# Optimization experiments

Measured on AMD Instinct MI355X. Metric: run time of the kernel, lower is better.

The kernel has to match this reference:

```python
import jax, jax.numpy as jnp
import numpy as np

B, T_ENC, T_DEC, E = 16, 512, 128, 512
H = 1024


def setup_inputs() -> dict:
    key = jax.random.key(0)
    ks = jax.random.split(key, 16)
    def rn(k, shape, s=0.02):
        return jax.random.normal(k, shape, jnp.float32) * s
    z = lambda *s: jnp.zeros(s, jnp.float32)
    return {
        "inputs": jax.random.normal(ks[0], (B, T_ENC, E), jnp.float32),
        "padded_mels": jax.random.normal(ks[1], (B, 80, T_DEC), jnp.float32),
        "W_enc": rn(ks[2], (128, E)),
        "W_q": rn(ks[3], (128, H)),
        "W_loc_conv": rn(ks[4], (32, 1, 31)),
        "b_loc_conv": z(32),
        "W_loc_dense": rn(ks[5], (128, 32)),
        "b_loc_dense": z(128),
        "w_e": rn(ks[6], (1, 128)),
        "b_e": z(1),
        "W_p1": rn(ks[7], (256, 80)),
        "W_p2": rn(ks[8], (256, 256)),
        "W_ih1": rn(ks[9], (4 * H, 256 + E)),
        "W_hh1": rn(ks[10], (4 * H, H)),
        "b_ih1": z(4 * H),
        "b_hh1": z(4 * H),
        "W_ih2": rn(ks[11], (4 * H, H)),
        "W_hh2": rn(ks[12], (4 * H, H)),
        "b_ih2": z(4 * H),
        "b_hh2": z(4 * H),
        "W_proj": rn(ks[13], (80, H + E)),
        "b_proj": z(80),
        "W_stop": rn(ks[14], (1, H + E)),
        "b_stop": z(1),
    }


def _lstm_cell(x, h, c, W_ih, W_hh, b_ih, b_hh):
    g = W_ih @ x + b_ih + W_hh @ h + b_hh
    i, f, gg, o = jnp.split(g, 4)  # torch gate order: i, f, g, o
    c = jax.nn.sigmoid(f) * c + jax.nn.sigmoid(i) * jnp.tanh(gg)
    h = jax.nn.sigmoid(o) * jnp.tanh(c)
    return h, c


def _forward(inputs, padded_mels, W_enc, W_q, W_loc_conv, b_loc_conv,
             W_loc_dense, b_loc_dense, w_e, b_e, W_p1, W_p2,
             W_ih1, W_hh1, b_ih1, b_hh1, W_ih2, W_hh2, b_ih2, b_hh2,
             W_proj, b_proj, W_stop, b_stop):
    proc_enc = inputs @ W_enc.T  # (B, T_enc, 128)
    # prepend zero frame, use frames 0..T_dec-1 as teacher-forced inputs
    prev = jnp.concatenate([jnp.zeros((B, 80, 1), inputs.dtype), padded_mels], axis=-1)[:, :, :T_DEC]
    prev = jnp.transpose(prev, (2, 0, 1))  # (T_dec, B, 80)
    # F.dropout(p=0.5) in source defaults to training=True -> always applied; deterministic masks here
    mk = jax.random.key(42)
    m1 = jax.random.bernoulli(jax.random.fold_in(mk, 0), 0.5, (T_DEC, B, 256)).astype(inputs.dtype) * 2.0
    m2 = jax.random.bernoulli(jax.random.fold_in(mk, 1), 0.5, (T_DEC, B, 256)).astype(inputs.dtype) * 2.0

    def lstm2(x_seq):
        # faithful to source: (B,1,768) fed to batch_first=False nn.LSTM ->
        # sequence runs over the batch dim with batch=1 and zero init state each step
        zv = jnp.zeros((H,), x_seq.dtype)
        def cell(carry, x):
            h1, c1, h2, c2 = carry
            h1, c1 = _lstm_cell(x, h1, c1, W_ih1, W_hh1, b_ih1, b_hh1)
            h2, c2 = _lstm_cell(h1, h2, c2, W_ih2, W_hh2, b_ih2, b_hh2)
            return (h1, c1, h2, c2), h2
        _, hs = jax.lax.scan(cell, (zv, zv, zv, zv), x_seq)
        return hs  # (B, 1024)

    def step(carry, xs):
        cum, ctx = carry  # (B, T_enc), (B, E)
        x, d1, d2 = xs
        p = jax.nn.relu(x @ W_p1.T) * d1
        p = jax.nn.relu(p @ W_p2.T) * d2
        h = lstm2(jnp.concatenate([p, ctx], axis=-1))  # (B, 1024)
        q = h @ W_q.T  # (B, 128)
        loc = jax.lax.conv_general_dilated(
            cum[:, None, :], W_loc_conv, (1,), [(15, 15)],
            dimension_numbers=("NCH", "OIH", "NCH")) + b_loc_conv[None, :, None]  # (B, 32, T_enc)
        loc = jnp.transpose(loc, (0, 2, 1)) @ W_loc_dense.T + b_loc_dense  # (B, T_enc, 128)
        e = jnp.tanh(q[:, None, :] + loc + proc_enc) @ w_e[0] + b_e[0]  # (B, T_enc)
        aw = jax.nn.softmax(e, axis=1)
        new_ctx = jnp.einsum("bt,bte->be", aw, inputs)  # (B, E)
        do = jnp.concatenate([h, new_ctx], axis=-1)  # (B, 1536)
        frame = do @ W_proj.T + b_proj  # (B, 80)
        stop = do @ W_stop[0] + b_stop[0]  # (B,)
        return (cum + aw, new_ctx), (frame, stop)

    carry0 = (jnp.zeros((B, T_ENC), inputs.dtype), jnp.zeros((B, E), inputs.dtype))
    _, (mels, stops) = jax.lax.scan(step, carry0, (prev, m1, m2))
    return jnp.transpose(mels, (1, 0, 2)), jnp.transpose(stops, (1, 0))


def reference(inputs, padded_mels, W_enc, W_q, W_loc_conv, b_loc_conv,
              W_loc_dense, b_loc_dense, w_e, b_e, W_p1, W_p2,
              W_ih1, W_hh1, b_ih1, b_hh1, W_ih2, W_hh2, b_ih2, b_hh2,
              W_proj, b_proj, W_stop, b_stop):
    return _forward(inputs, padded_mels, W_enc, W_q, W_loc_conv, b_loc_conv,
                    W_loc_dense, b_loc_dense, w_e, b_e, W_p1, W_p2,
                    W_ih1, W_hh1, b_ih1, b_hh1, W_ih2, W_hh2, b_ih2, b_hh2,
                    W_proj, b_proj, W_stop, b_stop)
```

## Files before the change

kernel.cpp:

```cpp
#include <hip/hip_runtime.h>
#include <hip/hip_bf16.h>
#include <stdint.h>

#define TD 128
#define NB 16
#define TE 512
#define EE 512
#define HH 1024
#define NM 80
#define PP 256
#define NWG 256
#define NTH 512

#define AGENT __HIP_MEMORY_SCOPE_AGENT

__device__ inline float aloadf(const float* p) {
  return __hip_atomic_load(p, __ATOMIC_RELAXED, AGENT);
}
__device__ inline void astoref(float* p, float v) {
  __hip_atomic_store(p, v, __ATOMIC_RELAXED, AGENT);
}
__device__ inline double aloadd(const double* p) {
  return __hip_atomic_load(p, __ATOMIC_RELAXED, AGENT);
}
__device__ inline void astored(double* p, double v) {
  __hip_atomic_store(p, v, __ATOMIC_RELAXED, AGENT);
}
__device__ inline float2 aload2f(const float* p) {
  unsigned long long v =
      __hip_atomic_load((const unsigned long long*)p, __ATOMIC_RELAXED, AGENT);
  union { unsigned long long u; float2 f; } c; c.u = v; return c.f;
}
__device__ inline double dsig(double x) { return 1.0 / (1.0 + exp(-x)); }

__host__ __device__ inline void threefry2x32(uint32_t k0, uint32_t k1,
                                             uint32_t& x0, uint32_t& x1) {
  uint32_t ks0 = k0, ks1 = k1, ks2 = k0 ^ k1 ^ 0x1BD11BDAu;
  x0 += ks0; x1 += ks1;
#define RND(rot) { x0 += x1; x1 = (x1 << (rot)) | (x1 >> (32 - (rot))); x1 ^= x0; }
  RND(13) RND(15) RND(26) RND(6)
  x0 += ks1; x1 += ks2 + 1u;
  RND(17) RND(29) RND(16) RND(24)
  x0 += ks2; x1 += ks0 + 2u;
  RND(13) RND(15) RND(26) RND(6)
  x0 += ks0; x1 += ks1 + 3u;
  RND(17) RND(29) RND(16) RND(24)
  x0 += ks1; x1 += ks2 + 4u;
  RND(13) RND(15) RND(26) RND(6)
  x0 += ks2; x1 += ks0 + 5u;
#undef RND
}

__device__ inline double mask_val(uint32_t ka, uint32_t kb, uint32_t i) {
  uint32_t x0 = 0u, x1 = i;
  threefry2x32(ka, kb, x0, x1);
  uint32_t bits = x0 ^ x1;
  float u = __uint_as_float((bits >> 9) | 0x3f800000u) - 1.0f;
  return (u < 0.5f) ? 2.0 : 0.0;
}

__global__ void k_proc_enc(const float* __restrict__ inputs,
                           const float* __restrict__ W_enc,
                           float* __restrict__ procTf) {
  int blk = blockIdx.x;
  int b = blk >> 5;
  int t0 = (blk & 31) * 16;
  int d = threadIdx.x;
  __shared__ float in_l[16][EE];
  for (int idx = threadIdx.x; idx < 16 * EE; idx += blockDim.x) {
    int tt = idx >> 9, e = idx & 511;
    in_l[tt][e] = inputs[((size_t)(b * TE + t0 + tt)) * EE + e];
  }
  __syncthreads();
  double acc[16];
#pragma unroll
  for (int tt = 0; tt < 16; ++tt) acc[tt] = 0.0;
  const float* wr = W_enc + (size_t)d * EE;
  for (int e = 0; e < EE; ++e) {
    double w = (double)wr[e];
#pragma unroll
    for (int tt = 0; tt < 16; ++tt) acc[tt] += w * (double)in_l[tt][e];
  }
  for (int tt = 0; tt < 16; ++tt)
    procTf[((size_t)(b * 128 + d)) * TE + t0 + tt] = (float)acc[tt];
}

__global__ void k_p(const float* __restrict__ pm, const float* __restrict__ Wp1,
                    const float* __restrict__ Wp2,
                    uint32_t k1a, uint32_t k1b, uint32_t k2a, uint32_t k2b,
                    float* __restrict__ p_allf) {
  int sb = blockIdx.x;
  int s = sb >> 4, b = sb & 15;
  int tid = threadIdx.x;
  uint32_t mi = (uint32_t)(sb * PP + tid);
  double d1 = mask_val(k1a, k1b, mi);
  double d2 = mask_val(k2a, k2b, mi);
  __shared__ float x_l[NM];
  __shared__ double p1_l[PP];
  if (tid < NM) x_l[tid] = (s == 0) ? 0.f : pm[(b * NM + tid) * TD + (s - 1)];
  __syncthreads();
  double a = 0.0;
  const float* w1 = Wp1 + tid * NM;
  for (int m = 0; m < NM; ++m) a += (double)w1[m] * (double)x_l[m];
  a = fmax(a, 0.0) * d1;
  p1_l[tid] = a;
  __syncthreads();
  double c = 0.0;
  const float* w2 = Wp2 + tid * PP;
  for (int k = 0; k < PP; ++k) c += (double)w2[k] * p1_l[k];
  c = fmax(c, 0.0) * d2;
  p_allf[sb * PP + tid] = (float)c;
}

__global__ void k_init(double* __restrict__ cumg, float* __restrict__ ctxf,
                       float* __restrict__ h1f, float* __restrict__ h2f,
                       uint32_t* __restrict__ barmem) {
  int tid = threadIdx.x;
  for (int i = tid; i < NB * TE; i += 256) cumg[i] = 0.0;
  for (int i = tid; i < NB * EE; i += 256) ctxf[i] = 0.f;
  for (int i = tid; i < 2 * HH; i += 256) { h1f[i] = 0.f; h2f[i] = 0.f; }
  for (int i = tid; i < 8320; i += 256) barmem[i] = 0u;
}

struct SMEM {
  float wldT[4096];
  float wcl[992];
  double bld[128], we[128], blc[32];
  double b1l[16], b2l[16];
  double g1l[16][16];
  double gA[16], gBC[16];
  double c1l[4], c2l[4];
  double be0;
  union U {
    struct { float h1[1024], h2[1024]; } cell;
    struct { float h[1024]; } pq;
    struct { float ctxall[8192]; } g1p;
    struct { double cum[64], q[128], loc[32][33]; } att;
    struct { float aw[512]; double red[16][32]; } ctxp;
    struct { double red[16]; } soft;
    struct { float hb[1536]; double red[16]; } outp;
  } u;
};

__device__ inline void gridbar(uint32_t* barmem, uint32_t& lgen, int wg, int tid) {
  __syncthreads();
  lgen++;
  if (wg == 0) {
    if (tid < 255) {
      const uint32_t* fl = &barmem[(tid + 1) * 16];
      while (__hip_atomic_load(fl, __ATOMIC_RELAXED, AGENT) < lgen)
        __builtin_amdgcn_s_sleep(1);
    }
    __syncthreads();
    if (tid == 0) {
      asm volatile("s_waitcnt vmcnt(0)" ::: "memory");
      __hip_atomic_store(&barmem[8192], lgen, __ATOMIC_RELAXED, AGENT);
    }
  } else {
    if (tid == 0) {
      __hip_atomic_store(&barmem[wg * 16], lgen, __ATOMIC_RELAXED, AGENT);
      while (__hip_atomic_load(&barmem[8192], __ATOMIC_RELAXED, AGENT) < lgen)
        __builtin_amdgcn_s_sleep(1);
    }
  }
  __syncthreads();
}

__global__ __launch_bounds__(NTH)
__attribute__((amdgpu_waves_per_eu(2, 2)))
void k_persist(
    const float* __restrict__ inputs,
    const float* __restrict__ W_q,
    const float* __restrict__ W_lc, const float* __restrict__ b_lc,
    const float* __restrict__ W_ld, const float* __restrict__ b_ld,
    const float* __restrict__ w_e, const float* __restrict__ b_e,
    const float* __restrict__ W_ih1, const float* __restrict__ W_hh1,
    const float* __restrict__ b_ih1, const float* __restrict__ b_hh1,
    const float* __restrict__ W_ih2, const float* __restrict__ W_hh2,
    const float* __restrict__ b_ih2, const float* __restrict__ b_hh2,
    const float* __restrict__ W_proj, const float* __restrict__ b_proj,
    const float* __restrict__ W_stop, const float* __restrict__ b_stop,
    const float* __restrict__ p_allf, const float* __restrict__ procTf,
    float* h1f, float* h2f, float* h_allf, float* qf,
    float* ef, float* awf, double* cumg, float* ctxf,
    uint32_t* barmem, float* out) {
  __shared__ SMEM sm;
  const int wg = blockIdx.x, tid = threadIdx.x;
  const int q = tid >> 5, l = tid & 31;
  const int row = (q >> 2) * 1024 + wg * 4 + (q & 3);
  uint32_t lgen = 0;

  for (int i = tid; i < 4096; i += NTH) sm.wldT[(i & 31) * 128 + (i >> 5)] = W_ld[i];
  for (int i = tid; i < 992; i += NTH) sm.wcl[i] = W_lc[i];
  for (int i = tid; i < 128; i += NTH) { sm.bld[i] = (double)b_ld[i]; sm.we[i] = (double)w_e[i]; }
  if (tid < 32) sm.blc[tid] = (double)b_lc[tid];
  if (tid == 0) sm.be0 = (double)b_e[0];
  if (l == 0) {
    sm.b1l[q] = (double)b_ih1[row] + (double)b_hh1[row];
    sm.b2l[q] = (double)b_ih2[row] + (double)b_hh2[row];
  }

  float wA[32], wB[32], wC[32], wD[24];
#pragma unroll
  for (int k = 0; k < 32; ++k) {
    int c = l + 32 * k;
    wA[k] = W_hh1[(size_t)row * 1024 + c];
    wB[k] = W_ih2[(size_t)row * 1024 + c];
    wC[k] = W_hh2[(size_t)row * 1024 + c];
  }
#pragma unroll
  for (int k = 0; k < 24; ++k) wD[k] = W_ih1[(size_t)row * 768 + l + 32 * k];
#pragma unroll
  for (int k = 0; k < 32; ++k) {
    asm volatile("" : "+v"(wA[k]));
    asm volatile("" : "+v"(wB[k]));
    asm volatile("" : "+v"(wC[k]));
  }
#pragma unroll
  for (int k = 0; k < 24; ++k) asm volatile("" : "+v"(wD[k]));
  __syncthreads();

  {
    for (int i = tid; i < 8192; i += NTH) sm.u.g1p.ctxall[i] = aloadf(ctxf + i);
    __syncthreads();
    for (int b = 0; b < 16; ++b) {
      double a = 0.0;
#pragma unroll
      for (int k = 0; k < 8; ++k)
        a += (double)wD[k] * (double)p_allf[((size_t)0 * 16 + b) * 256 + l + 32 * k];
#pragma unroll
      for (int k = 8; k < 24; ++k)
        a += (double)wD[k] * (double)sm.u.g1p.ctxall[b * 512 + l + 32 * k - 256];
#pragma unroll
      for (int m = 1; m <= 16; m <<= 1) a += __shfl_xor(a, m);
      if (l == 0) sm.g1l[b][q] = a + sm.b1l[q];
    }
    __syncthreads();
  }
  gridbar(barmem, lgen, wg, tid);

  for (int s = 0; s < TD; ++s) {
    for (int r = 0; r <= 16; ++r) {
      if (r == 0 && tid < 4) { sm.c1l[tid] = 0.0; sm.c2l[tid] = 0.0; }
      {
        float2 v1 = aload2f(h1f + (((r & 1) ^ 1)) * 1024 + 2 * tid);
        sm.u.cell.h1[2 * tid] = v1.x; sm.u.cell.h1[2 * tid + 1] = v1.y;
        if (r > 0) {
          float2 v2 = aload2f(h2f + (r & 1) * 1024 + 2 * tid);
          sm.u.cell.h2[2 * tid] = v2.x; sm.u.cell.h2[2 * tid + 1] = v2.y;
        }
      }
      __syncthreads();

      double a0 = 0.0, a1 = 0.0, a2 = 0.0;
#pragma unroll
      for (int k = 0; k < 32; ++k) {
        double h1v = (double)sm.u.cell.h1[l + 32 * k];
        a0 += (double)wA[k] * h1v;
        a1 += (double)wB[k] * h1v;
        a2 += (double)wC[k] * (double)sm.u.cell.h2[l + 32 * k];
      }
#pragma unroll
      for (int m = 1; m <= 16; m <<= 1) {
        a0 += __shfl_xor(a0, m);
        a1 += __shfl_xor(a1, m);
        a2 += __shfl_xor(a2, m);
      }
      if (l == 0) { sm.gA[q] = a0; sm.gBC[q] = a1 + a2; }
      __syncthreads();

      if (r < 16 && tid < 4) {
        int jj = tid;
        double gi = sm.g1l[r][jj]      + sm.gA[jj];
        double gf = sm.g1l[r][4 + jj]  + sm.gA[4 + jj];
        double gg = sm.g1l[r][8 + jj]  + sm.gA[8 + jj];
        double go = sm.g1l[r][12 + jj] + sm.gA[12 + jj];
        double cn = dsig(gf) * sm.c1l[jj] + dsig(gi) * tanh(gg);
        double hn = dsig(go) * tanh(cn);
        sm.c1l[jj] = cn;
        astoref(h1f + (r & 1) * 1024 + wg * 4 + jj, (float)hn);
      }
      if (r > 0 && tid >= 8 && tid < 12) {
        int jj = tid - 8, b = r - 1;
        double gi = sm.gBC[jj]      + sm.b2l[jj];
        double gf = sm.gBC[4 + jj]  + sm.b2l[4 + jj];
        double gg = sm.gBC[8 + jj]  + sm.b2l[8 + jj];
        double go = sm.gBC[12 + jj] + sm.b2l[12 + jj];
        double cn = dsig(gf) * sm.c2l[jj] + dsig(gi) * tanh(gg);
        double hn = dsig(go) * tanh(cn);
        sm.c2l[jj] = cn;
        astoref(h2f + ((b & 1)) * 1024 + wg * 4 + jj, (float)hn);
        astoref(h_allf + (size_t)b * 1024 + wg * 4 + jj, (float)hn);
      }
      gridbar(barmem, lgen, wg, tid);
    }

    {
      int b = wg >> 4;
      float2 v = aload2f(h_allf + (size_t)b * 1024 + 2 * tid);
      sm.u.pq.h[2 * tid] = v.x; sm.u.pq.h[2 * tid + 1] = v.y;
      __syncthreads();
      int o = tid >> 6, lane = tid & 63;
      int d = (wg & 15) * 8 + o;
      double a = 0.0;
#pragma unroll
      for (int k = 0; k < 16; ++k) {
        int c = lane + 64 * k;
        a += (double)W_q[(size_t)d * 1024 + c] * (double)sm.u.pq.h[c];
      }
#pragma unroll
      for (int m = 1; m <= 32; m <<= 1) a += __shfl_xor(a, m);
      if (lane == 0) astoref(qf + b * 128 + d, (float)a);
    }
    gridbar(barmem, lgen, wg, tid);

    {
      int b = wg >> 4, t0 = (wg & 15) * 32;
      if (tid < 62) {
        int g = t0 - 15 + tid;
        sm.u.att.cum[tid] = (g >= 0 && g < TE) ? aloadd(cumg + b * TE + g) : 0.0;
      } else if (tid < 190) {
        sm.u.att.q[tid - 62] = (double)aloadf(qf + b * 128 + (tid - 62));
      }
      __syncthreads();
#pragma unroll
      for (int it = 0; it < 2; ++it) {
        int task = tid + it * NTH;
        int t = task >> 5, ch = task & 31;
        double v = sm.blc[ch];
#pragma unroll
        for (int k = 0; k < 31; ++k) v += (double)sm.wcl[ch * 31 + k] * sm.u.att.cum[t + k];
        sm.u.att.loc[t][ch] = v;
      }
      __syncthreads();
      int t = tid >> 4, part = tid & 15;
      double en = 0.0;
      for (int k = 0; k < 8; ++k) {
        int d = part + 16 * k;
        double sv = sm.u.att.q[d] + sm.bld[d] +
                    (double)procTf[((size_t)(b * 128 + d)) * TE + t0 + t];
#pragma unroll
        for (int c = 0; c < 32; ++c)
          sv += sm.u.att.loc[t][c] * (double)sm.wldT[c * 128 + d];
        en += tanh(sv) * sm.we[d];
      }
#pragma unroll
      for (int m = 1; m <= 8; m <<= 1) en += __shfl_xor(en, m);
      if (part == 0) astoref(ef + b * TE + t0 + t, (float)(en + sm.be0));
    }
    gridbar(barmem, lgen, wg, tid);

    if (wg < 16) {
      int b = wg;
      double e = (double)aloadf(ef + b * TE + tid);
      double mx = e;
#pragma unroll
      for (int m = 1; m <= 32; m <<= 1) mx = fmax(mx, __shfl_xor(mx, m));
      if ((tid & 63) == 0) sm.u.soft.red[tid >> 6] = mx;
      __syncthreads();
      if (tid == 0) {
        double mm = sm.u.soft.red[0];
        for (int i = 1; i < 8; ++i) mm = fmax(mm, sm.u.soft.red[i]);
        sm.u.soft.red[0] = mm;
      }
      __syncthreads();
      double p = exp(e - sm.u.soft.red[0]);
      __syncthreads();
      double ssum = p;
#pragma unroll
      for (int m = 1; m <= 32; m <<= 1) ssum += __shfl_xor(ssum, m);
      if ((tid & 63) == 0) sm.u.soft.red[tid >> 6] = ssum;
      __syncthreads();
      if (tid == 0) {
        double t_ = 0.0;
        for (int i = 0; i < 8; ++i) t_ += sm.u.soft.red[i];
        sm.u.soft.red[0] = 1.0 / t_;
      }
      __syncthreads();
      double a = p * sm.u.soft.red[0];
      astoref(awf + b * TE + tid, (float)a);
      astored(cumg + b * TE + tid, aloadd(cumg + b * TE + tid) + a);
    }
    gridbar(barmem, lgen, wg, tid);

    {
      int b = wg >> 4, e0 = (wg & 15) * 32;
      sm.u.ctxp.aw[tid] = aloadf(awf + b * TE + tid);
      __syncthreads();
      int e = e0 + (tid & 31), tp = tid >> 5;
      double a = 0.0;
      for (int t = tp * 32; t < tp * 32 + 32; ++t)
        a += (double)sm.u.ctxp.aw[t] * (double)inputs[((size_t)(b * TE + t)) * EE + e];
      sm.u.ctxp.red[tp][tid & 31] = a;
      __syncthreads();
      if (tid < 32) {
        double v = 0.0;
        for (int j = 0; j < 16; ++j) v += sm.u.ctxp.red[j][tid];
        astoref(ctxf + b * EE + e0 + tid, (float)v);
      }
    }
    gridbar(barmem, lgen, wg, tid);

    {
      int b = wg & 15, obase = wg >> 4;
      for (int i = tid; i < 1536; i += NTH)
        sm.u.outp.hb[i] = (i < 1024) ? aloadf(h_allf + (size_t)b * 1024 + i)
                                     : aloadf(ctxf + b * EE + (i - 1024));
      __syncthreads();
      for (int j = 0; j < 6; ++j) {
        int o = obase + 16 * j;
        if (o <= NM) {
          const float* wr = (o < NM) ? (W_proj + (size_t)o * 1536) : W_stop;
          double a = 0.0;
#pragma unroll
          for (int kk = 0; kk < 3; ++kk) {
            int k = tid + kk * NTH;
            a += (double)wr[k] * (double)sm.u.outp.hb[k];
          }
#pragma unroll
          for (int m = 1; m <= 32; m <<= 1) a += __shfl_xor(a, m);
          if ((tid & 63) == 0) sm.u.outp.red[tid >> 6] = a;
          __syncthreads();
          if (tid == 0) {
            double v = 0.0;
            for (int i = 0; i < 8; ++i) v += sm.u.outp.red[i];
            v += (o < NM) ? (double)b_proj[o] : (double)b_stop[0];
            if (o < NM) out[((size_t)b * TD + s) * NM + o] = (float)v;
            else        out[(size_t)NB * TD * NM + b * TD + s] = (float)v;
          }
          __syncthreads();
        }
      }
      __syncthreads();
      if (s < TD - 1) {
        const int ss = s + 1;
        for (int i = tid; i < 8192; i += NTH) sm.u.g1p.ctxall[i] = aloadf(ctxf + i);
        __syncthreads();
        for (int b2 = 0; b2 < 16; ++b2) {
          double a = 0.0;
#pragma unroll
          for (int k = 0; k < 8; ++k)
            a += (double)wD[k] * (double)p_allf[((size_t)ss * 16 + b2) * 256 + l + 32 * k];
#pragma unroll
          for (int k = 8; k < 24; ++k)
            a += (double)wD[k] * (double)sm.u.g1p.ctxall[b2 * 512 + l + 32 * k - 256];
#pragma unroll
          for (int m = 1; m <= 16; m <<= 1) a += __shfl_xor(a, m);
          if (l == 0) sm.g1l[b2][q] = a + sm.b1l[q];
        }
        __syncthreads();
        if (tid < 4) astoref(h1f + 1024 + wg * 4 + tid, 0.f);
        else if (tid < 8) astoref(h2f + 1024 + wg * 4 + (tid - 4), 0.f);
      }
    }
    gridbar(barmem, lgen, wg, tid);
  }
}

extern "C" void kernel_launch(void* const* d_in, const int* in_sizes, int n_in,
                              void* d_out, int out_size, void* d_ws, size_t ws_size,
                              hipStream_t stream) {
  const float* inputs = (const float*)d_in[0];
  const float* pmels  = (const float*)d_in[1];
  const float* W_enc  = (const float*)d_in[2];
  const float* W_q    = (const float*)d_in[3];
  const float* W_lc   = (const float*)d_in[4];
  const float* b_lc   = (const float*)d_in[5];
  const float* W_ld   = (const float*)d_in[6];
  const float* b_ld   = (const float*)d_in[7];
  const float* w_e    = (const float*)d_in[8];
  const float* b_e    = (const float*)d_in[9];
  const float* W_p1   = (const float*)d_in[10];
  const float* W_p2   = (const float*)d_in[11];
  const float* W_ih1  = (const float*)d_in[12];
  const float* W_hh1  = (const float*)d_in[13];
  const float* b_ih1  = (const float*)d_in[14];
  const float* b_hh1  = (const float*)d_in[15];
  const float* W_ih2  = (const float*)d_in[16];
  const float* W_hh2  = (const float*)d_in[17];
  const float* b_ih2  = (const float*)d_in[18];
  const float* b_hh2  = (const float*)d_in[19];
  const float* W_proj = (const float*)d_in[20];
  const float* b_proj = (const float*)d_in[21];
  const float* W_stop = (const float*)d_in[22];
  const float* b_stop = (const float*)d_in[23];
  float* out = (float*)d_out;

  float* ws     = (float*)d_ws;
  float* p_allf = ws;
  float* procTf = p_allf + 524288;
  float* h1f    = procTf + 1048576;
  float* h2f    = h1f + 2048;
  float* h_allf = h2f + 2048;
  float* qf     = h_allf + 16384;
  float* ef     = qf + 2048;
  float* awf    = ef + 8192;
  float* ctxf   = awf + 8192;
  double* cumg  = (double*)(ctxf + 8192);
  uint32_t* barmem = (uint32_t*)(cumg + 8192);

  uint32_t k1a = 0u, k1b = 0u, k2a = 0u, k2b = 1u;
  threefry2x32(0u, 42u, k1a, k1b);
  threefry2x32(0u, 42u, k2a, k2b);

  k_proc_enc<<<512, 128, 0, stream>>>(inputs, W_enc, procTf);
  k_p<<<TD * NB, 256, 0, stream>>>(pmels, W_p1, W_p2, k1a, k1b, k2a, k2b, p_allf);
  k_init<<<1, 256, 0, stream>>>(cumg, ctxf, h1f, h2f, barmem);

  k_persist<<<NWG, NTH, 0, stream>>>(
      inputs, W_q, W_lc, b_lc, W_ld, b_ld, w_e, b_e,
      W_ih1, W_hh1, b_ih1, b_hh1, W_ih2, W_hh2, b_ih2, b_hh2,
      W_proj, b_proj, W_stop, b_stop,
      p_allf, procTf, h1f, h2f, h_allf, qf, ef, awf, cumg, ctxf,
      barmem, out);

  (void)in_sizes; (void)n_in; (void)out_size; (void)ws_size;
}
```

Measured before the change: 34.28 ms.

## Fuse query projection and softmax into neighbors to drop grid barriers

Each workgroup now computes the query projection redundantly inside the attention-energy phase, and recomputes the softmax locally inside the context phase. This removes two grid-wide barriers and the global round-trips for q and attention weights in every decoder step. The grid barrier release also switches from a single shared flag to per-workgroup flags, so waiters poll distinct cache lines. The cost is redundant W_q and softmax arithmetic in every workgroup.

```diff
diff --git a/kernel.cpp b/kernel.cpp
--- a/kernel.cpp
+++ b/kernel.cpp
@@ -119,7 +119,7 @@
   for (int i = tid; i < NB * TE; i += 256) cumg[i] = 0.0;
   for (int i = tid; i < NB * EE; i += 256) ctxf[i] = 0.f;
   for (int i = tid; i < 2 * HH; i += 256) { h1f[i] = 0.f; h2f[i] = 0.f; }
-  for (int i = tid; i < 8320; i += 256) barmem[i] = 0u;
+  for (int i = tid; i < 8192; i += 256) barmem[i] = 0u;
 }
 
 struct SMEM {
@@ -133,11 +133,9 @@
   double be0;
   union U {
     struct { float h1[1024], h2[1024]; } cell;
-    struct { float h[1024]; } pq;
     struct { float ctxall[8192]; } g1p;
-    struct { double cum[64], q[128], loc[32][33]; } att;
-    struct { float aw[512]; double red[16][32]; } ctxp;
-    struct { double red[16]; } soft;
+    struct { float h[1024]; double cum[64], q[128], loc[32][33]; } att;
+    struct { float aw[512]; double red[16][32]; double red8[8]; } ctxp;
     struct { float hb[1536]; double red[16]; } outp;
   } u;
 };
@@ -146,20 +144,20 @@
   __syncthreads();
   lgen++;
   if (wg == 0) {
-    if (tid < 255) {
-      const uint32_t* fl = &barmem[(tid + 1) * 16];
+    if (tid >= 256 && tid < 511) {
+      const uint32_t* fl = &barmem[(tid - 255) * 16];
       while (__hip_atomic_load(fl, __ATOMIC_RELAXED, AGENT) < lgen)
         __builtin_amdgcn_s_sleep(1);
     }
     __syncthreads();
-    if (tid == 0) {
+    if (tid < 256) {
       asm volatile("s_waitcnt vmcnt(0)" ::: "memory");
-      __hip_atomic_store(&barmem[8192], lgen, __ATOMIC_RELAXED, AGENT);
+      __hip_atomic_store(&barmem[4096 + tid * 16], lgen, __ATOMIC_RELAXED, AGENT);
     }
   } else {
     if (tid == 0) {
       __hip_atomic_store(&barmem[wg * 16], lgen, __ATOMIC_RELAXED, AGENT);
-      while (__hip_atomic_load(&barmem[8192], __ATOMIC_RELAXED, AGENT) < lgen)
+      while (__hip_atomic_load(&barmem[4096 + wg * 16], __ATOMIC_RELAXED, AGENT) < lgen)
         __builtin_amdgcn_s_sleep(1);
     }
   }
@@ -181,8 +179,8 @@
     const float* __restrict__ W_proj, const float* __restrict__ b_proj,
     const float* __restrict__ W_stop, const float* __restrict__ b_stop,
     const float* __restrict__ p_allf, const float* __restrict__ procTf,
-    float* h1f, float* h2f, float* h_allf, float* qf,
-    float* ef, float* awf, double* cumg, float* ctxf,
+    float* h1f, float* h2f, float* h_allf,
+    float* ef, double* cumg, float* ctxf,
     uint32_t* barmem, float* out) {
   __shared__ SMEM sm;
   const int wg = blockIdx.x, tid = threadIdx.x;
@@ -296,33 +294,25 @@
     }
 
     {
-      int b = wg >> 4;
-      float2 v = aload2f(h_allf + (size_t)b * 1024 + 2 * tid);
-      sm.u.pq.h[2 * tid] = v.x; sm.u.pq.h[2 * tid + 1] = v.y;
-      __syncthreads();
-      int o = tid >> 6, lane = tid & 63;
-      int d = (wg & 15) * 8 + o;
-      double a = 0.0;
-#pragma unroll
-      for (int k = 0; k < 16; ++k) {
-        int c = lane + 64 * k;
-        a += (double)W_q[(size_t)d * 1024 + c] * (double)sm.u.pq.h[c];
-      }
-#pragma unroll
-      for (int m = 1; m <= 32; m <<= 1) a += __shfl_xor(a, m);
-      if (lane == 0) astoref(qf + b * 128 + d, (float)a);
-    }
-    gridbar(barmem, lgen, wg, tid);
-
-    {
       int b = wg >> 4, t0 = (wg & 15) * 32;
+      {
+        float2 v = aload2f(h_allf + (size_t)b * 1024 + 2 * tid);
+        sm.u.att.h[2 * tid] = v.x; sm.u.att.h[2 * tid + 1] = v.y;
+      }
       if (tid < 62) {
         int g = t0 - 15 + tid;
         sm.u.att.cum[tid] = (g >= 0 && g < TE) ? aloadd(cumg + b * TE + g) : 0.0;
-      } else if (tid < 190) {
-        sm.u.att.q[tid - 62] = (double)aloadf(qf + b * 128 + (tid - 62));
-      }
-      __syncthreads();
+      }
+      __syncthreads();
+      {
+        int d = tid >> 2, sub = tid & 3;
+        const float* wq = W_q + (size_t)d * 1024 + sub * 256;
+        const float* hh = sm.u.att.h + sub * 256;
+        double a = 0.0;
+        for (int k = 0; k < 256; ++k) a += (double)wq[k] * (double)hh[k];
+        a += __shfl_xor(a, 1); a += __shfl_xor(a, 2);
+        if (sub == 0) sm.u.att.q[d] = a;
+      }
 #pragma unroll
       for (int it = 0; it < 2; ++it) {
         int task = tid + it * NTH;
@@ -350,48 +340,43 @@
     }
     gridbar(barmem, lgen, wg, tid);
 
-    if (wg < 16) {
-      int b = wg;
+    {
+      int b = wg >> 4, e0 = (wg & 15) * 32;
       double e = (double)aloadf(ef + b * TE + tid);
       double mx = e;
 #pragma unroll
       for (int m = 1; m <= 32; m <<= 1) mx = fmax(mx, __shfl_xor(mx, m));
-      if ((tid & 63) == 0) sm.u.soft.red[tid >> 6] = mx;
+      if ((tid & 63) == 0) sm.u.ctxp.red8[tid >> 6] = mx;
       __syncthreads();
       if (tid == 0) {
-        double mm = sm.u.soft.red[0];
-        for (int i = 1; i < 8; ++i) mm = fmax(mm, sm.u.soft.red[i]);
-        sm.u.soft.red[0] = mm;
-      }
-      __syncthreads();
-      double p = exp(e - sm.u.soft.red[0]);
+        double mm = sm.u.ctxp.red8[0];
+        for (int i = 1; i < 8; ++i) mm = fmax(mm, sm.u.ctxp.red8[i]);
+        sm.u.ctxp.red8[0] = mm;
+      }
+      __syncthreads();
+      double p = exp(e - sm.u.ctxp.red8[0]);
       __syncthreads();
       double ssum = p;
 #pragma unroll
       for (int m = 1; m <= 32; m <<= 1) ssum += __shfl_xor(ssum, m);
-      if ((tid & 63) == 0) sm.u.soft.red[tid >> 6] = ssum;
+      if ((tid & 63) == 0) sm.u.ctxp.red8[tid >> 6] = ssum;
       __syncthreads();
       if (tid == 0) {
         double t_ = 0.0;
-        for (int i = 0; i < 8; ++i) t_ += sm.u.soft.red[i];
-        sm.u.soft.red[0] = 1.0 / t_;
-      }
-      __syncthreads();
-      double a = p * sm.u.soft.red[0];
-      astoref(awf + b * TE + tid, (float)a);
-      astored(cumg + b * TE + tid, aloadd(cumg + b * TE + tid) + a);
-    }
-    gridbar(barmem, lgen, wg, tid);
-
-    {
-      int b = wg >> 4, e0 = (wg & 15) * 32;
-      sm.u.ctxp.aw[tid] = aloadf(awf + b * TE + tid);
-      __syncthreads();
-      int e = e0 + (tid & 31), tp = tid >> 5;
-      double a = 0.0;
+        for (int i = 0; i < 8; ++i) t_ += sm.u.ctxp.red8[i];
+        sm.u.ctxp.red8[0] = 1.0 / t_;
+      }
+      __syncthreads();
+      double a = p * sm.u.ctxp.red8[0];
+      sm.u.ctxp.aw[tid] = (float)a;
+      if ((wg & 15) == 0)
+        astored(cumg + b * TE + tid, aloadd(cumg + b * TE + tid) + a);
+      __syncthreads();
+      int e2 = e0 + (tid & 31), tp = tid >> 5;
+      double acc = 0.0;
       for (int t = tp * 32; t < tp * 32 + 32; ++t)
-        a += (double)sm.u.ctxp.aw[t] * (double)inputs[((size_t)(b * TE + t)) * EE + e];
-      sm.u.ctxp.red[tp][tid & 31] = a;
+        acc += (double)sm.u.ctxp.aw[t] * (double)inputs[((size_t)(b * TE + t)) * EE + e2];
+      sm.u.ctxp.red[tp][tid & 31] = acc;
       __syncthreads();
       if (tid < 32) {
         double v = 0.0;
@@ -492,10 +477,8 @@
   float* h1f    = procTf + 1048576;
   float* h2f    = h1f + 2048;
   float* h_allf = h2f + 2048;
-  float* qf     = h_allf + 16384;
-  float* ef     = qf + 2048;
-  float* awf    = ef + 8192;
-  float* ctxf   = awf + 8192;
+  float* ef     = h_allf + 16384;
+  float* ctxf   = ef + 8192;
   double* cumg  = (double*)(ctxf + 8192);
   uint32_t* barmem = (uint32_t*)(cumg + 8192);
 
@@ -511,7 +494,7 @@
       inputs, W_q, W_lc, b_lc, W_ld, b_ld, w_e, b_e,
       W_ih1, W_hh1, b_ih1, b_hh1, W_ih2, W_hh2, b_ih2, b_hh2,
       W_proj, b_proj, W_stop, b_stop,
-      p_allf, procTf, h1f, h2f, h_allf, qf, ef, awf, cumg, ctxf,
+      p_allf, procTf, h1f, h2f, h_allf, ef, cumg, ctxf,
       barmem, out);
 
   (void)in_sizes; (void)n_in; (void)out_size; (void)ws_size;
```

Result: slower. 41.90 ms (+22.3%).

## Widen cross-workgroup loads, use sc0 inline asm, and parallelize barrier release

Applied to the files above, without the earlier changes.

Replaces relaxed atomic scalar/float2 loads of shared state with 128-bit global loads carrying the sc0 cache bit via inline asm, so each exchange of hidden state and context needs fewer memory transactions. The grid barrier now has workgroup 0 release all waiters in parallel through per-workgroup flags instead of one shared flag, which removes contention on a single spinning address. Acquire loads are added for ordering. The risk is that memory ordering now depends on the sc0 cache semantics and the explicit waitcnt inside each asm load, which also serializes those loads.

```diff
diff --git a/kernel.cpp b/kernel.cpp
--- a/kernel.cpp
+++ b/kernel.cpp
@@ -14,22 +14,31 @@
 
 #define AGENT __HIP_MEMORY_SCOPE_AGENT
 
-__device__ inline float aloadf(const float* p) {
-  return __hip_atomic_load(p, __ATOMIC_RELAXED, AGENT);
-}
+typedef float f32x4 __attribute__((ext_vector_type(4)));
+
 __device__ inline void astoref(float* p, float v) {
   __hip_atomic_store(p, v, __ATOMIC_RELAXED, AGENT);
 }
-__device__ inline double aloadd(const double* p) {
-  return __hip_atomic_load(p, __ATOMIC_RELAXED, AGENT);
-}
 __device__ inline void astored(double* p, double v) {
   __hip_atomic_store(p, v, __ATOMIC_RELAXED, AGENT);
 }
-__device__ inline float2 aload2f(const float* p) {
-  unsigned long long v =
-      __hip_atomic_load((const unsigned long long*)p, __ATOMIC_RELAXED, AGENT);
-  union { unsigned long long u; float2 f; } c; c.u = v; return c.f;
+__device__ inline f32x4 ntload4(const float* p) {
+  f32x4 r;
+  asm volatile("global_load_dwordx4 %0, %1, off sc0\n\ts_waitcnt vmcnt(0)"
+               : "=&v"(r) : "v"(p) : "memory");
+  return r;
+}
+__device__ inline float ntload1f(const float* p) {
+  float r;
+  asm volatile("global_load_dword %0, %1, off sc0\n\ts_waitcnt vmcnt(0)"
+               : "=&v"(r) : "v"(p) : "memory");
+  return r;
+}
+__device__ inline double ntload1d(const double* p) {
+  double r;
+  asm volatile("global_load_dwordx2 %0, %1, off sc0\n\ts_waitcnt vmcnt(0)"
+               : "=&v"(r) : "v"(p) : "memory");
+  return r;
 }
 __device__ inline double dsig(double x) { return 1.0 / (1.0 + exp(-x)); }
 
@@ -119,7 +128,7 @@
   for (int i = tid; i < NB * TE; i += 256) cumg[i] = 0.0;
   for (int i = tid; i < NB * EE; i += 256) ctxf[i] = 0.f;
   for (int i = tid; i < 2 * HH; i += 256) { h1f[i] = 0.f; h2f[i] = 0.f; }
-  for (int i = tid; i < 8320; i += 256) barmem[i] = 0u;
+  for (int i = tid; i < 8192; i += 256) barmem[i] = 0u;
 }
 
 struct SMEM {
@@ -146,20 +155,23 @@
   __syncthreads();
   lgen++;
   if (wg == 0) {
-    if (tid < 255) {
-      const uint32_t* fl = &barmem[(tid + 1) * 16];
+    if (tid == 0)
+      (void)__hip_atomic_load(&barmem[0], __ATOMIC_ACQUIRE, AGENT);
+    if (tid >= 256 && tid < 511) {
+      const uint32_t* fl = &barmem[(tid - 255) * 16];
       while (__hip_atomic_load(fl, __ATOMIC_RELAXED, AGENT) < lgen)
         __builtin_amdgcn_s_sleep(1);
     }
     __syncthreads();
-    if (tid == 0) {
+    if (tid < 256) {
       asm volatile("s_waitcnt vmcnt(0)" ::: "memory");
-      __hip_atomic_store(&barmem[8192], lgen, __ATOMIC_RELAXED, AGENT);
+      __hip_atomic_store(&barmem[4096 + tid * 16], lgen, __ATOMIC_RELAXED, AGENT);
     }
   } else {
     if (tid == 0) {
+      (void)__hip_atomic_load(&barmem[wg * 16], __ATOMIC_ACQUIRE, AGENT);
       __hip_atomic_store(&barmem[wg * 16], lgen, __ATOMIC_RELAXED, AGENT);
-      while (__hip_atomic_load(&barmem[8192], __ATOMIC_RELAXED, AGENT) < lgen)
+      while (__hip_atomic_load(&barmem[4096 + wg * 16], __ATOMIC_RELAXED, AGENT) < lgen)
         __builtin_amdgcn_s_sleep(1);
     }
   }
@@ -221,7 +233,10 @@
   __syncthreads();
 
   {
-    for (int i = tid; i < 8192; i += NTH) sm.u.g1p.ctxall[i] = aloadf(ctxf + i);
+    for (int j = 0; j < 4; ++j) {
+      f32x4 v = ntload4(ctxf + (tid + j * NTH) * 4);
+      *(f32x4*)&sm.u.g1p.ctxall[(tid + j * NTH) * 4] = v;
+    }
     __syncthreads();
     for (int b = 0; b < 16; ++b) {
       double a = 0.0;
@@ -242,13 +257,12 @@
   for (int s = 0; s < TD; ++s) {
     for (int r = 0; r <= 16; ++r) {
       if (r == 0 && tid < 4) { sm.c1l[tid] = 0.0; sm.c2l[tid] = 0.0; }
-      {
-        float2 v1 = aload2f(h1f + (((r & 1) ^ 1)) * 1024 + 2 * tid);
-        sm.u.cell.h1[2 * tid] = v1.x; sm.u.cell.h1[2 * tid + 1] = v1.y;
-        if (r > 0) {
-          float2 v2 = aload2f(h2f + (r & 1) * 1024 + 2 * tid);
-          sm.u.cell.h2[2 * tid] = v2.x; sm.u.cell.h2[2 * tid + 1] = v2.y;
-        }
+      if (tid < 256) {
+        f32x4 v = ntload4(h1f + (((r & 1) ^ 1)) * 1024 + tid * 4);
+        *(f32x4*)&sm.u.cell.h1[tid * 4] = v;
+      } else if (r > 0) {
+        f32x4 v = ntload4(h2f + (r & 1) * 1024 + (tid - 256) * 4);
+        *(f32x4*)&sm.u.cell.h2[(tid - 256) * 4] = v;
       }
       __syncthreads();
 
@@ -297,8 +311,10 @@
 
     {
       int b = wg >> 4;
-      float2 v = aload2f(h_allf + (size_t)b * 1024 + 2 * tid);
-      sm.u.pq.h[2 * tid] = v.x; sm.u.pq.h[2 * tid + 1] = v.y;
+      if (tid < 256) {
+        f32x4 v = ntload4(h_allf + (size_t)b * 1024 + tid * 4);
+        *(f32x4*)&sm.u.pq.h[tid * 4] = v;
+      }
       __syncthreads();
       int o = tid >> 6, lane = tid & 63;
       int d = (wg & 15) * 8 + o;
@@ -318,9 +334,9 @@
       int b = wg >> 4, t0 = (wg & 15) * 32;
       if (tid < 62) {
         int g = t0 - 15 + tid;
-        sm.u.att.cum[tid] = (g >= 0 && g < TE) ? aloadd(cumg + b * TE + g) : 0.0;
+        sm.u.att.cum[tid] = (g >= 0 && g < TE) ? ntload1d(cumg + b * TE + g) : 0.0;
       } else if (tid < 190) {
-        sm.u.att.q[tid - 62] = (double)aloadf(qf + b * 128 + (tid - 62));
+        sm.u.att.q[tid - 62] = (double)ntload1f(qf + b * 128 + (tid - 62));
       }
       __syncthreads();
 #pragma unroll
@@ -352,7 +368,7 @@
 
     if (wg < 16) {
       int b = wg;
-      double e = (double)aloadf(ef + b * TE + tid);
+      double e = (double)ntload1f(ef + b * TE + tid);
       double mx = e;
 #pragma unroll
       for (int m = 1; m <= 32; m <<= 1) mx = fmax(mx, __shfl_xor(mx, m));
@@ -379,13 +395,13 @@
       __syncthreads();
       double a = p * sm.u.soft.red[0];
       astoref(awf + b * TE + tid, (float)a);
-      astored(cumg + b * TE + tid, aloadd(cumg + b * TE + tid) + a);
+      astored(cumg + b * TE + tid, ntload1d(cumg + b * TE + tid) + a);
     }
     gridbar(barmem, lgen, wg, tid);
 
     {
       int b = wg >> 4, e0 = (wg & 15) * 32;
-      sm.u.ctxp.aw[tid] = aloadf(awf + b * TE + tid);
+      sm.u.ctxp.aw[tid] = ntload1f(awf + b * TE + tid);
       __syncthreads();
       int e = e0 + (tid & 31), tp = tid >> 5;
       double a = 0.0;
@@ -403,9 +419,13 @@
 
     {
       int b = wg & 15, obase = wg >> 4;
-      for (int i = tid; i < 1536; i += NTH)
-        sm.u.outp.hb[i] = (i < 1024) ? aloadf(h_allf + (size_t)b * 1024 + i)
-                                     : aloadf(ctxf + b * EE + (i - 1024));
+      if (tid < 256) {
+        f32x4 v = ntload4(h_allf + (size_t)b * 1024 + tid * 4);
+        *(f32x4*)&sm.u.outp.hb[tid * 4] = v;
+      } else if (tid < 384) {
+        f32x4 v = ntload4(ctxf + b * EE + (tid - 256) * 4);
+        *(f32x4*)&sm.u.outp.hb[1024 + (tid - 256) * 4] = v;
+      }
       __syncthreads();
       for (int j = 0; j < 6; ++j) {
         int o = obase + 16 * j;
@@ -425,8 +445,8 @@
             double v = 0.0;
             for (int i = 0; i < 8; ++i) v += sm.u.outp.red[i];
             v += (o < NM) ? (double)b_proj[o] : (double)b_stop[0];
-            if (o < NM) out[((size_t)b * TD + s) * NM + o] = (float)v;
-            else        out[(size_t)NB * TD * NM + b * TD + s] = (float)v;
+            if (o < NM) astoref(out + ((size_t)b * TD + s) * NM + o, (float)v);
+            else        astoref(out + (size_t)NB * TD * NM + b * TD + s, (float)v);
           }
           __syncthreads();
         }
@@ -434,7 +454,10 @@
       __syncthreads();
       if (s < TD - 1) {
         const int ss = s + 1;
-        for (int i = tid; i < 8192; i += NTH) sm.u.g1p.ctxall[i] = aloadf(ctxf + i);
+        for (int j = 0; j < 4; ++j) {
+          f32x4 v = ntload4(ctxf + (tid + j * NTH) * 4);
+          *(f32x4*)&sm.u.g1p.ctxall[(tid + j * NTH) * 4] = v;
+        }
         __syncthreads();
         for (int b2 = 0; b2 < 16; ++b2) {
           double a = 0.0;
```

Result: no change. 33.80 ms (-1.4%).
